# Kernel optimization log

Measured on AMD Instinct MI355X. Metric: run time of the kernel, lower is better.

The kernel has to match this reference:

```python
import jax, jax.numpy as jnp
import numpy as np

N, H, S, D = 2, 8, 2048, 64

def setup_inputs() -> dict:
    key = jax.random.key(0)
    k1, k2, k3, k4 = jax.random.split(key, 4)
    queries = jax.random.normal(k1, (N, H, S, D), dtype=jnp.float32)
    keys = jax.random.normal(k2, (N, H, S, D), dtype=jnp.float32)
    values = jax.random.normal(k3, (N, H, S, D), dtype=jnp.float32)
    attn_mask = jax.random.randint(k4, (1, 1, S, S), 0, 2, dtype=jnp.int32)
    return {"queries": queries, "keys": keys, "values": values, "attn_mask": attn_mask}

def reference(queries, keys, values, attn_mask):
    # Faithful to the torch code: softmax over axis=2 (query/seq axis) for Q,
    # softmax over axis=1 (heads axis) for K, exactly as written.
    Q = jax.nn.softmax(queries, axis=2)
    K = jax.nn.softmax(keys, axis=1)
    attention_weights = jnp.einsum('nhqd,nhkd->nhqk', Q, K)  # [N,H,S,S]
    attention_weights = jnp.where(attn_mask == 0, -jnp.inf, attention_weights)
    attention_weights = jax.nn.softmax(attention_weights, axis=-1)
    context = jnp.einsum('nhqk,nhkd->nhqd', attention_weights, values)
    return context, attention_weights
```

## Files before the change

kernel.cpp:

```cpp
#include <hip/hip_runtime.h>

#define S 2048
#define Dh 64
#define NH 16
#define SD (S*Dh)
#define SSZ ((size_t)S*(size_t)S)

typedef __attribute__((ext_vector_type(4))) float f32x4;
typedef __attribute__((ext_vector_type(8))) short s16x8;

#define WSB_QSUM 0
#define WSB_MASK 4096
#define WSB_QS   (4096 + 524288)
#define WSB_KS   (WSB_QS + 4194304)
#define WSB_VT   (WSB_KS + 4194304)

__device__ __forceinline__ ushort f2bf(float x) {
    unsigned u = __builtin_bit_cast(unsigned, x);
    u = (u + 0x7fffu + ((u >> 16) & 1u)) >> 16;
    return (ushort)u;
}

__global__ void k_qsum(const float* __restrict__ q, float* __restrict__ qsum) {
    const int head  = blockIdx.x >> 3;
    const int chunk = blockIdx.x & 7;
    const int t = threadIdx.x;
    const int d = t & 63, sg = t >> 6;
    const float* qh = q + (size_t)head * SD;
    const int s0 = chunk * 256;
    float acc = 0.f;
#pragma unroll 8
    for (int i = 0; i < 64; ++i) {
        int s = s0 + sg + 4 * i;
        acc += __expf(qh[s * Dh + d]);
    }
    __shared__ float part[4][64];
    part[sg][d] = acc;
    __syncthreads();
    if (sg == 0)
        atomicAdd(&qsum[head * 64 + d], part[0][d] + part[1][d] + part[2][d] + part[3][d]);
}

__global__ void k_qnorm(const float* __restrict__ q, const float* __restrict__ qsum,
                        ushort* __restrict__ Qs) {
    const int gid = blockIdx.x * 256 + threadIdx.x;
    const int i0 = gid * 8;
    const int head = i0 >> 17;
    const int d0 = i0 & 63;
    const float4 a = ((const float4*)(q + i0))[0];
    const float4 b = ((const float4*)(q + i0))[1];
    const float* qs = qsum + head * 64 + d0;
    s16x8 o;
    o[0] = (short)f2bf(__expf(a.x) / qs[0]);
    o[1] = (short)f2bf(__expf(a.y) / qs[1]);
    o[2] = (short)f2bf(__expf(a.z) / qs[2]);
    o[3] = (short)f2bf(__expf(a.w) / qs[3]);
    o[4] = (short)f2bf(__expf(b.x) / qs[4]);
    o[5] = (short)f2bf(__expf(b.y) / qs[5]);
    o[6] = (short)f2bf(__expf(b.z) / qs[6]);
    o[7] = (short)f2bf(__expf(b.w) / qs[7]);
    *(s16x8*)(Qs + i0) = o;
}

__global__ void k_ksoft(const float* __restrict__ kin, ushort* __restrict__ Ks) {
    const int gid = blockIdx.x * 256 + threadIdx.x;
    const int n = gid >> 17;
    const int rem = gid & (SD - 1);
    const float* base = kin + (size_t)n * 8 * SD + rem;
    float x[8];
    float sum = 0.f;
#pragma unroll
    for (int h = 0; h < 8; ++h) { x[h] = __expf(base[(size_t)h * SD]); sum += x[h]; }
    const float inv = 1.f / sum;
    ushort* ob = Ks + (size_t)n * 8 * SD + rem;
#pragma unroll
    for (int h = 0; h < 8; ++h) ob[(size_t)h * SD] = f2bf(x[h] * inv);
}

__global__ void k_vt(const float* __restrict__ V, ushort* __restrict__ Vt) {
    const int head = blockIdx.x >> 5, kt = blockIdx.x & 31;
    const int t = threadIdx.x;
    __shared__ float sv[64 * 68];
    const float4* src = (const float4*)(V + (size_t)head * SD + (size_t)kt * 64 * 64);
#pragma unroll
    for (int i = 0; i < 4; ++i) {
        int idx = t + 256 * i;
        int row = idx >> 4, c4 = idx & 15;
        *(float4*)&sv[row * 68 + c4 * 4] = src[idx];
    }
    __syncthreads();
    const int d = t >> 2, seg = t & 3;
    s16x8 v0, v1;
#pragma unroll
    for (int j = 0; j < 8; ++j) v0[j] = (short)f2bf(sv[(seg * 16 + j) * 68 + d]);
#pragma unroll
    for (int j = 0; j < 8; ++j) v1[j] = (short)f2bf(sv[(seg * 16 + 8 + j) * 68 + d]);
    ushort* dst = Vt + (size_t)head * SD + (size_t)d * S + kt * 64 + seg * 16;
    *(s16x8*)dst = v0;
    *(s16x8*)(dst + 8) = v1;
}

__global__ void k_mask(const int* __restrict__ mask, unsigned long long* __restrict__ bm) {
    const int t = threadIdx.x;
    const int g = blockIdx.x * 4 + (t >> 6);
    const int lane = t & 63;
    for (int it = 0; it < 64; ++it) {
        int w = g * 64 + it;
        int m = mask[(size_t)w * 64 + lane];
        unsigned long long b = __ballot(m != 0);
        if (lane == 0) bm[w] = b;
    }
}

#define LB 72
#define LF 68
__global__ __launch_bounds__(256, 4) void k_attn(
        const ushort* __restrict__ Qs, const ushort* __restrict__ Ks,
        const ushort* __restrict__ Vt, const unsigned long long* __restrict__ bm,
        float* __restrict__ ctx, float* __restrict__ A) {
    const int qt = blockIdx.x, head = blockIdx.y;
    const int q0 = qt * 64;
    const int t = threadIdx.x;
    const int lane = t & 63, wv = t >> 6;
    const int lm = lane & 15, lg = lane >> 4;

    __shared__ __align__(16) char smem[37376];
    ushort* sQ = (ushort*)smem;
    ushort* sK = (ushort*)(smem + 9216);
    ushort* sV = (ushort*)(smem + 18432);
    ushort* sP = (ushort*)(smem + 27648);
    unsigned long long* sM = (unsigned long long*)(smem + 36864);
    float* sPf = (float*)(smem + 18432);

    {
        const s16x8* src = (const s16x8*)(Qs + (size_t)head * SD + (size_t)q0 * 64);
#pragma unroll
        for (int i = 0; i < 2; ++i) {
            int idx = t + 256 * i;
            int row = idx >> 3, seg = idx & 7;
            *(s16x8*)&sQ[row * LB + seg * 8] = src[idx];
        }
    }

    f32x4 o[4];
#pragma unroll
    for (int c = 0; c < 4; ++c) o[c] = (f32x4){0.f, 0.f, 0.f, 0.f};
    float rs[4] = {0.f, 0.f, 0.f, 0.f};

    const ushort* Kbase = Ks + (size_t)head * SD;
    const ushort* Vbase = Vt + (size_t)head * SD;

    for (int kt = 0; kt < 32; ++kt) {
        const int k0 = kt * 64;
        __syncthreads();
#pragma unroll
        for (int i = 0; i < 2; ++i) {
            int idx = t + 256 * i;
            int row = idx >> 3, seg = idx & 7;
            *(s16x8*)&sK[row * LB + seg * 8] = *(const s16x8*)(Kbase + (size_t)(k0 + row) * 64 + seg * 8);
            *(s16x8*)&sV[row * LB + seg * 8] = *(const s16x8*)(Vbase + (size_t)row * S + k0 + seg * 8);
        }
        if (t < 64) sM[t] = bm[(size_t)(q0 + t) * 32 + kt];
        __syncthreads();

        f32x4 sc[4];
#pragma unroll
        for (int c = 0; c < 4; ++c) sc[c] = (f32x4){0.f, 0.f, 0.f, 0.f};
#pragma unroll
        for (int h = 0; h < 2; ++h) {
            s16x8 aq = *(const s16x8*)&sQ[(16 * wv + lm) * LB + 32 * h + 8 * lg];
#pragma unroll
            for (int c = 0; c < 4; ++c) {
                s16x8 bk = *(const s16x8*)&sK[(16 * c + lm) * LB + 32 * h + 8 * lg];
                sc[c] = __builtin_amdgcn_mfma_f32_16x16x32_bf16(aq, bk, sc[c], 0, 0, 0);
            }
        }
#pragma unroll
        for (int r = 0; r < 4; ++r) {
            const int rowl = 16 * wv + 4 * lg + r;
            const unsigned long long m64 = sM[rowl];
            float rsum = 0.f;
#pragma unroll
            for (int c = 0; c < 4; ++c) {
                float p = ((m64 >> (16 * c + lm)) & 1ULL) ? __expf(sc[c][r]) : 0.f;
                rsum += p;
                sP[rowl * LB + 16 * c + lm] = f2bf(p);
            }
            rsum += __shfl_xor(rsum, 1);
            rsum += __shfl_xor(rsum, 2);
            rsum += __shfl_xor(rsum, 4);
            rsum += __shfl_xor(rsum, 8);
            rs[r] += rsum;
        }
        __syncthreads();
#pragma unroll
        for (int h = 0; h < 2; ++h) {
            s16x8 ap = *(const s16x8*)&sP[(16 * wv + lm) * LB + 32 * h + 8 * lg];
#pragma unroll
            for (int c = 0; c < 4; ++c) {
                s16x8 bv = *(const s16x8*)&sV[(16 * c + lm) * LB + 32 * h + 8 * lg];
                o[c] = __builtin_amdgcn_mfma_f32_16x16x32_bf16(ap, bv, o[c], 0, 0, 0);
            }
        }
    }

    float inv[4];
#pragma unroll
    for (int r = 0; r < 4; ++r) inv[r] = 1.f / rs[r];

#pragma unroll
    for (int r = 0; r < 4; ++r) {
        const int qrow = q0 + 16 * wv + 4 * lg + r;
        float* cb = ctx + (size_t)head * SD + (size_t)qrow * 64;
#pragma unroll
        for (int c = 0; c < 4; ++c) cb[16 * c + lm] = o[c][r] * inv[r];
    }

    float* Abase = A + (size_t)head * SSZ;
    for (int kt = 0; kt < 32; ++kt) {
        const int k0 = kt * 64;
        __syncthreads();
#pragma unroll
        for (int i = 0; i < 2; ++i) {
            int idx = t + 256 * i;
            int row = idx >> 3, seg = idx & 7;
            *(s16x8*)&sK[row * LB + seg * 8] = *(const s16x8*)(Kbase + (size_t)(k0 + row) * 64 + seg * 8);
        }
        if (t < 64) sM[t] = bm[(size_t)(q0 + t) * 32 + kt];
        __syncthreads();

        f32x4 sc[4];
#pragma unroll
        for (int c = 0; c < 4; ++c) sc[c] = (f32x4){0.f, 0.f, 0.f, 0.f};
#pragma unroll
        for (int h = 0; h < 2; ++h) {
            s16x8 aq = *(const s16x8*)&sQ[(16 * wv + lm) * LB + 32 * h + 8 * lg];
#pragma unroll
            for (int c = 0; c < 4; ++c) {
                s16x8 bk = *(const s16x8*)&sK[(16 * c + lm) * LB + 32 * h + 8 * lg];
                sc[c] = __builtin_amdgcn_mfma_f32_16x16x32_bf16(aq, bk, sc[c], 0, 0, 0);
            }
        }
#pragma unroll
        for (int r = 0; r < 4; ++r) {
            const int rowl = 16 * wv + 4 * lg + r;
            const unsigned long long m64 = sM[rowl];
#pragma unroll
            for (int c = 0; c < 4; ++c) {
                float p = ((m64 >> (16 * c + lm)) & 1ULL) ? __expf(sc[c][r]) * inv[r] : 0.f;
                sPf[rowl * LF + 16 * c + lm] = p;
            }
        }
        __syncthreads();
#pragma unroll
        for (int i = 0; i < 4; ++i) {
            int idx = t + 256 * i;
            int row = idx >> 4, c4 = idx & 15;
            *(float4*)&Abase[(size_t)(q0 + row) * S + k0 + c4 * 4] = *(const float4*)&sPf[row * LF + c4 * 4];
        }
    }
}

extern "C" void kernel_launch(void* const* d_in, const int* in_sizes, int n_in,
                              void* d_out, int out_size, void* d_ws, size_t ws_size,
                              hipStream_t stream) {
    const float* q = (const float*)d_in[0];
    const float* k = (const float*)d_in[1];
    const float* v = (const float*)d_in[2];
    const int* mask = (const int*)d_in[3];
    float* out = (float*)d_out;
    char* ws = (char*)d_ws;

    float* qsum = (float*)(ws + WSB_QSUM);
    unsigned long long* bm = (unsigned long long*)(ws + WSB_MASK);
    ushort* Qs = (ushort*)(ws + WSB_QS);
    ushort* Ks = (ushort*)(ws + WSB_KS);
    ushort* Vt = (ushort*)(ws + WSB_VT);

    hipMemsetAsync(d_ws, 0, 4096, stream);
    k_qsum<<<128, 256, 0, stream>>>(q, qsum);
    k_mask<<<256, 256, 0, stream>>>(mask, bm);
    k_qnorm<<<1024, 256, 0, stream>>>(q, qsum, Qs);
    k_ksoft<<<1024, 256, 0, stream>>>(k, Ks);
    k_vt<<<512, 256, 0, stream>>>(v, Vt);
    k_attn<<<dim3(32, 16), 256, 0, stream>>>(Qs, Ks, Vt, bm,
                                             out, out + (size_t)NH * SD);
}
```

Baseline: 419.5 us.

## Split attention into context kernel and parallel attention-weights writer kernel

```diff
diff --git a/kernel.cpp b/kernel.cpp
--- a/kernel.cpp
+++ b/kernel.cpp
@@ -10,8 +10,9 @@
 typedef __attribute__((ext_vector_type(8))) short s16x8;
 
 #define WSB_QSUM 0
-#define WSB_MASK 4096
-#define WSB_QS   (4096 + 524288)
+#define WSB_RINV 4096
+#define WSB_MASK 135168
+#define WSB_QS   659456
 #define WSB_KS   (WSB_QS + 4194304)
 #define WSB_VT   (WSB_KS + 4194304)
 
@@ -114,37 +115,36 @@
 
 #define LB 72
 #define LF 68
-__global__ __launch_bounds__(256, 4) void k_attn(
+
+__global__ __launch_bounds__(256, 4) void k_ctx(
         const ushort* __restrict__ Qs, const ushort* __restrict__ Ks,
         const ushort* __restrict__ Vt, const unsigned long long* __restrict__ bm,
-        float* __restrict__ ctx, float* __restrict__ A) {
+        float* __restrict__ ctx, float* __restrict__ rinv) {
     const int qt = blockIdx.x, head = blockIdx.y;
-    const int q0 = qt * 64;
+    const int q0 = qt * 32;
     const int t = threadIdx.x;
     const int lane = t & 63, wv = t >> 6;
     const int lm = lane & 15, lg = lane >> 4;
-
-    __shared__ __align__(16) char smem[37376];
+    const int wm = wv & 1;
+    const int wn = wv >> 1;
+
+    __shared__ __align__(16) char smem[28416];
     ushort* sQ = (ushort*)smem;
-    ushort* sK = (ushort*)(smem + 9216);
-    ushort* sV = (ushort*)(smem + 18432);
-    ushort* sP = (ushort*)(smem + 27648);
-    unsigned long long* sM = (unsigned long long*)(smem + 36864);
-    float* sPf = (float*)(smem + 18432);
+    ushort* sK = (ushort*)(smem + 4608);
+    ushort* sV = (ushort*)(smem + 13824);
+    ushort* sP = (ushort*)(smem + 23040);
+    unsigned long long* sM = (unsigned long long*)(smem + 27648);
+    float* sRS = (float*)(smem + 27904);
 
     {
         const s16x8* src = (const s16x8*)(Qs + (size_t)head * SD + (size_t)q0 * 64);
-#pragma unroll
-        for (int i = 0; i < 2; ++i) {
-            int idx = t + 256 * i;
-            int row = idx >> 3, seg = idx & 7;
-            *(s16x8*)&sQ[row * LB + seg * 8] = src[idx];
-        }
-    }
-
-    f32x4 o[4];
-#pragma unroll
-    for (int c = 0; c < 4; ++c) o[c] = (f32x4){0.f, 0.f, 0.f, 0.f};
+        int row = t >> 3, seg = t & 7;
+        *(s16x8*)&sQ[row * LB + seg * 8] = src[t];
+    }
+
+    f32x4 o[2];
+    o[0] = (f32x4){0.f, 0.f, 0.f, 0.f};
+    o[1] = (f32x4){0.f, 0.f, 0.f, 0.f};
     float rs[4] = {0.f, 0.f, 0.f, 0.f};
 
     const ushort* Kbase = Ks + (size_t)head * SD;
@@ -160,31 +160,32 @@
             *(s16x8*)&sK[row * LB + seg * 8] = *(const s16x8*)(Kbase + (size_t)(k0 + row) * 64 + seg * 8);
             *(s16x8*)&sV[row * LB + seg * 8] = *(const s16x8*)(Vbase + (size_t)row * S + k0 + seg * 8);
         }
-        if (t < 64) sM[t] = bm[(size_t)(q0 + t) * 32 + kt];
-        __syncthreads();
-
-        f32x4 sc[4];
-#pragma unroll
-        for (int c = 0; c < 4; ++c) sc[c] = (f32x4){0.f, 0.f, 0.f, 0.f};
+        if (t < 32) sM[t] = bm[(size_t)(q0 + t) * 32 + kt];
+        __syncthreads();
+
+        f32x4 sc[2];
+        sc[0] = (f32x4){0.f, 0.f, 0.f, 0.f};
+        sc[1] = (f32x4){0.f, 0.f, 0.f, 0.f};
 #pragma unroll
         for (int h = 0; h < 2; ++h) {
-            s16x8 aq = *(const s16x8*)&sQ[(16 * wv + lm) * LB + 32 * h + 8 * lg];
-#pragma unroll
-            for (int c = 0; c < 4; ++c) {
-                s16x8 bk = *(const s16x8*)&sK[(16 * c + lm) * LB + 32 * h + 8 * lg];
-                sc[c] = __builtin_amdgcn_mfma_f32_16x16x32_bf16(aq, bk, sc[c], 0, 0, 0);
+            s16x8 aq = *(const s16x8*)&sQ[(16 * wm + lm) * LB + 32 * h + 8 * lg];
+#pragma unroll
+            for (int j = 0; j < 2; ++j) {
+                s16x8 bk = *(const s16x8*)&sK[(16 * (2 * wn + j) + lm) * LB + 32 * h + 8 * lg];
+                sc[j] = __builtin_amdgcn_mfma_f32_16x16x32_bf16(aq, bk, sc[j], 0, 0, 0);
             }
         }
 #pragma unroll
         for (int r = 0; r < 4; ++r) {
-            const int rowl = 16 * wv + 4 * lg + r;
+            const int rowl = 16 * wm + 4 * lg + r;
             const unsigned long long m64 = sM[rowl];
             float rsum = 0.f;
 #pragma unroll
-            for (int c = 0; c < 4; ++c) {
-                float p = ((m64 >> (16 * c + lm)) & 1ULL) ? __expf(sc[c][r]) : 0.f;
+            for (int j = 0; j < 2; ++j) {
+                const int col = 16 * (2 * wn + j) + lm;
+                float p = ((m64 >> col) & 1ULL) ? __expf(sc[j][r]) : 0.f;
                 rsum += p;
-                sP[rowl * LB + 16 * c + lm] = f2bf(p);
+                sP[rowl * LB + col] = f2bf(p);
             }
             rsum += __shfl_xor(rsum, 1);
             rsum += __shfl_xor(rsum, 2);
@@ -193,32 +194,75 @@
             rs[r] += rsum;
         }
         __syncthreads();
+
 #pragma unroll
         for (int h = 0; h < 2; ++h) {
-            s16x8 ap = *(const s16x8*)&sP[(16 * wv + lm) * LB + 32 * h + 8 * lg];
-#pragma unroll
-            for (int c = 0; c < 4; ++c) {
-                s16x8 bv = *(const s16x8*)&sV[(16 * c + lm) * LB + 32 * h + 8 * lg];
-                o[c] = __builtin_amdgcn_mfma_f32_16x16x32_bf16(ap, bv, o[c], 0, 0, 0);
-            }
-        }
-    }
-
-    float inv[4];
-#pragma unroll
-    for (int r = 0; r < 4; ++r) inv[r] = 1.f / rs[r];
+            s16x8 ap = *(const s16x8*)&sP[(16 * wm + lm) * LB + 32 * h + 8 * lg];
+#pragma unroll
+            for (int j = 0; j < 2; ++j) {
+                s16x8 bv = *(const s16x8*)&sV[(16 * (2 * wn + j) + lm) * LB + 32 * h + 8 * lg];
+                o[j] = __builtin_amdgcn_mfma_f32_16x16x32_bf16(ap, bv, o[j], 0, 0, 0);
+            }
+        }
+    }
+
+    if (lm == 0) {
+#pragma unroll
+        for (int r = 0; r < 4; ++r)
+            sRS[(16 * wm + 4 * lg + r) * 2 + wn] = rs[r];
+    }
+    __syncthreads();
+    if (t < 32) {
+        float inv = 1.f / (sRS[t * 2] + sRS[t * 2 + 1]);
+        rinv[head * S + q0 + t] = inv;
+        sRS[t * 2] = inv;
+    }
+    __syncthreads();
 
 #pragma unroll
     for (int r = 0; r < 4; ++r) {
-        const int qrow = q0 + 16 * wv + 4 * lg + r;
-        float* cb = ctx + (size_t)head * SD + (size_t)qrow * 64;
-#pragma unroll
-        for (int c = 0; c < 4; ++c) cb[16 * c + lm] = o[c][r] * inv[r];
-    }
-
+        const int rowl = 16 * wm + 4 * lg + r;
+        const float inv = sRS[rowl * 2];
+        float* cb = ctx + (size_t)head * SD + (size_t)(q0 + rowl) * 64;
+#pragma unroll
+        for (int j = 0; j < 2; ++j)
+            cb[16 * (2 * wn + j) + lm] = o[j][r] * inv;
+    }
+}
+
+__global__ __launch_bounds__(256, 4) void k_awrite(
+        const ushort* __restrict__ Qs, const ushort* __restrict__ Ks,
+        const unsigned long long* __restrict__ bm, const float* __restrict__ rinv,
+        float* __restrict__ A) {
+    const int qt = blockIdx.x, head = blockIdx.y, kc = blockIdx.z;
+    const int q0 = qt * 64;
+    const int t = threadIdx.x;
+    const int lane = t & 63, wv = t >> 6;
+    const int lm = lane & 15, lg = lane >> 4;
+
+    __shared__ __align__(16) char smem[36608];
+    ushort* sQ = (ushort*)smem;
+    ushort* sK = (ushort*)(smem + 9216);
+    float* sPf = (float*)(smem + 18432);
+    unsigned long long* sM = (unsigned long long*)(smem + 35840);
+    float* sI = (float*)(smem + 36352);
+
+    {
+        const s16x8* src = (const s16x8*)(Qs + (size_t)head * SD + (size_t)q0 * 64);
+#pragma unroll
+        for (int i = 0; i < 2; ++i) {
+            int idx = t + 256 * i;
+            int row = idx >> 3, seg = idx & 7;
+            *(s16x8*)&sQ[row * LB + seg * 8] = src[idx];
+        }
+        if (t < 64) sI[t] = rinv[head * S + q0 + t];
+    }
+
+    const ushort* Kbase = Ks + (size_t)head * SD;
     float* Abase = A + (size_t)head * SSZ;
-    for (int kt = 0; kt < 32; ++kt) {
-        const int k0 = kt * 64;
+
+    for (int kt8 = 0; kt8 < 8; ++kt8) {
+        const int k0 = kc * 512 + kt8 * 64;
         __syncthreads();
 #pragma unroll
         for (int i = 0; i < 2; ++i) {
@@ -226,7 +270,7 @@
             int row = idx >> 3, seg = idx & 7;
             *(s16x8*)&sK[row * LB + seg * 8] = *(const s16x8*)(Kbase + (size_t)(k0 + row) * 64 + seg * 8);
         }
-        if (t < 64) sM[t] = bm[(size_t)(q0 + t) * 32 + kt];
+        if (t < 64) sM[t] = bm[(size_t)(q0 + t) * 32 + (k0 >> 6)];
         __syncthreads();
 
         f32x4 sc[4];
@@ -245,10 +289,11 @@
         for (int r = 0; r < 4; ++r) {
             const int rowl = 16 * wv + 4 * lg + r;
             const unsigned long long m64 = sM[rowl];
+            const float invr = sI[rowl];
 #pragma unroll
             for (int c = 0; c < 4; ++c) {
-                float p = ((m64 >> (16 * c + lm)) & 1ULL) ? __expf(sc[c][r]) * inv[r] : 0.f;
-                sPf[rowl * LF + 16 * c + lm] = p;
+                const int col = 16 * c + lm;
+                sPf[rowl * LF + col] = ((m64 >> col) & 1ULL) ? __expf(sc[c][r]) * invr : 0.f;
             }
         }
         __syncthreads();
@@ -272,6 +317,7 @@
     char* ws = (char*)d_ws;
 
     float* qsum = (float*)(ws + WSB_QSUM);
+    float* rinv = (float*)(ws + WSB_RINV);
     unsigned long long* bm = (unsigned long long*)(ws + WSB_MASK);
     ushort* Qs = (ushort*)(ws + WSB_QS);
     ushort* Ks = (ushort*)(ws + WSB_KS);
@@ -283,6 +329,6 @@
     k_qnorm<<<1024, 256, 0, stream>>>(q, qsum, Qs);
     k_ksoft<<<1024, 256, 0, stream>>>(k, Ks);
     k_vt<<<512, 256, 0, stream>>>(v, Vt);
-    k_attn<<<dim3(32, 16), 256, 0, stream>>>(Qs, Ks, Vt, bm,
-                                             out, out + (size_t)NH * SD);
-}
+    k_ctx<<<dim3(64, 16), 256, 0, stream>>>(Qs, Ks, Vt, bm, out, rinv);
+    k_awrite<<<dim3(32, 16, 4), 256, 0, stream>>>(Qs, Ks, bm, rinv, out + (size_t)NH * SD);
+}
```

New measurement: 431.3 us. 1.03x slower.
